# Kernel tuning notes

Hardware: AMD Instinct MI355X
Metric: run time of the kernel (lower is better)

The kernel has to match this reference:

```python
import jax, jax.numpy as jnp
import numpy as np

N = 100000   # nodes
E = 1600000  # edges
EPS = 1e-5   # BatchNorm eps

def setup_inputs() -> dict:
    key = jax.random.key(0)
    ks = jax.random.split(key, 18)
    x = jax.random.normal(ks[0], (N, 128), jnp.float32)
    edge_index = jax.random.randint(ks[1], (2, E), 0, N, dtype=jnp.int64)
    # GCN layer weights (Glorot-ish scale) and biases
    W1 = jax.random.normal(ks[2], (128, 64), jnp.float32) * 0.1
    b1 = jnp.zeros((64,), jnp.float32)
    W2 = jax.random.normal(ks[3], (64, 64), jnp.float32) * 0.1
    b2 = jnp.zeros((64,), jnp.float32)
    W3 = jax.random.normal(ks[4], (64, 16), jnp.float32) * 0.1
    b3 = jnp.zeros((16,), jnp.float32)
    # BatchNorm (eval mode) affine params + running stats, 2 BN layers of width 64
    g1 = jax.random.uniform(ks[5], (64,), jnp.float32, 0.5, 1.5)
    be1 = jax.random.normal(ks[6], (64,), jnp.float32) * 0.1
    m1 = jax.random.normal(ks[7], (64,), jnp.float32) * 0.1
    v1 = jax.random.uniform(ks[8], (64,), jnp.float32, 0.5, 1.5)
    g2 = jax.random.uniform(ks[9], (64,), jnp.float32, 0.5, 1.5)
    be2 = jax.random.normal(ks[10], (64,), jnp.float32) * 0.1
    m2 = jax.random.normal(ks[11], (64,), jnp.float32) * 0.1
    v2 = jax.random.uniform(ks[12], (64,), jnp.float32, 0.5, 1.5)
    return {"x": x, "edge_index": edge_index,
            "W1": W1, "b1": b1, "W2": W2, "b2": b2, "W3": W3, "b3": b3,
            "g1": g1, "be1": be1, "m1": m1, "v1": v1,
            "g2": g2, "be2": be2, "m2": m2, "v2": v2}

def _gcn_graph(edge_index):
    # add self-loops, compute symmetric normalization deg^-1/2 * deg^-1/2
    loop = jnp.arange(N, dtype=edge_index.dtype)
    src = jnp.concatenate([edge_index[0], loop])
    dst = jnp.concatenate([edge_index[1], loop])
    deg = jax.ops.segment_sum(jnp.ones_like(dst, dtype=jnp.float32), dst, num_segments=N)
    dinv = jnp.where(deg > 0, jax.lax.rsqrt(jnp.maximum(deg, 1.0)), 0.0)
    norm = dinv[src] * dinv[dst]  # [E+N]
    return src, dst, norm

def reference(x, edge_index, W1, b1, W2, b2, W3, b3,
              g1, be1, m1, v1, g2, be2, m2, v2):
    src, dst, norm = _gcn_graph(edge_index)

    def conv(h, W, b):
        h = h @ W                              # [N, d_out]
        msg = h[src] * norm[:, None]           # gather + scale, [E+N, d_out]
        return jax.ops.segment_sum(msg, dst, num_segments=N) + b

    def bn(h, g, be, m, v):
        return g * (h - m) * jax.lax.rsqrt(v + EPS) + be

    h = jax.nn.relu(bn(conv(x, W1, b1), g1, be1, m1, v1))
    h = jax.nn.relu(bn(conv(h, W2, b2), g2, be2, m2, v2))
    return jax.nn.sigmoid(conv(h, W3, b3))
```

## Files before the change

kernel.cpp:

```cpp
#include <hip/hip_runtime.h>
#include <math.h>

#define NN 100000
#define NE 1600000
#define EPSBN 1e-5f
#define NBUCK 391

static __device__ __forceinline__ unsigned short f2bf(float f) {
    unsigned int u = __float_as_uint(f);
    u += 0x7fffu + ((u >> 16) & 1u);
    return (unsigned short)(u >> 16);
}
static __device__ __forceinline__ float bf2f(unsigned short s) {
    return __uint_as_float(((unsigned int)s) << 16);
}
static __device__ __forceinline__ float4 bf4_to_f4(ushort4 u) {
    float4 c; c.x = bf2f(u.x); c.y = bf2f(u.y); c.z = bf2f(u.z); c.w = bf2f(u.w);
    return c;
}
static __device__ __forceinline__ void add4(float4& a, float4 c) {
    a.x += c.x; a.y += c.y; a.z += c.z; a.w += c.w;
}
static __device__ __forceinline__ void fma4(float4& a, float s, const float4& w) {
    a.x = fmaf(s, w.x, a.x); a.y = fmaf(s, w.y, a.y);
    a.z = fmaf(s, w.z, a.z); a.w = fmaf(s, w.w, a.w);
}
static __device__ __forceinline__ void fma2(float2& a, float s, const float2& w) {
    a.x = fmaf(s, w.x, a.x); a.y = fmaf(s, w.y, a.y);
}

__global__ __launch_bounds__(512) void init_small(int* __restrict__ bkcnt,
                                                  int* __restrict__ bcur) {
    int t = threadIdx.x;
    bkcnt[t] = 0;
    bcur[t] = 0;
}

__global__ __launch_bounds__(256) void bucket_count(const int* __restrict__ dst,
                                                    int* __restrict__ bkcnt) {
    __shared__ int lh[NBUCK];
    int t = threadIdx.x;
    for (int b = t; b < NBUCK; b += 256) lh[b] = 0;
    __syncthreads();
    int e0 = blockIdx.x * 4096;
#pragma unroll
    for (int i = 0; i < 16; ++i) {
        int e = e0 + i * 256 + t;
        if (e < NE) atomicAdd(&lh[dst[e] >> 8], 1);
    }
    __syncthreads();
    for (int b = t; b < NBUCK; b += 256)
        if (lh[b]) atomicAdd(&bkcnt[b], lh[b]);
}

__global__ __launch_bounds__(512) void scan2(const int* __restrict__ bkcnt,
                                             int* __restrict__ bb0) {
    __shared__ int sh[512];
    int t = threadIdx.x;
    int val = (t < NBUCK) ? bkcnt[t] : 0;
    sh[t] = val;
    __syncthreads();
    for (int off = 1; off < 512; off <<= 1) {
        int x = (t >= off) ? sh[t - off] : 0;
        __syncthreads();
        sh[t] += x;
        __syncthreads();
    }
    bb0[t] = sh[t] - val;
}

__global__ __launch_bounds__(256) void bin_kernel(const int* __restrict__ src,
                                                  const int* __restrict__ dst,
                                                  const int* __restrict__ bb0,
                                                  int* __restrict__ bcur,
                                                  unsigned int* __restrict__ bucketed) {
    __shared__ int lh[NBUCK];
    __shared__ int lbase[NBUCK];
    __shared__ int lcur[NBUCK];
    int t = threadIdx.x;
    for (int b = t; b < NBUCK; b += 256) lh[b] = 0;
    __syncthreads();
    int e0 = blockIdx.x * 4096;
#pragma unroll
    for (int i = 0; i < 16; ++i) {
        int e = e0 + i * 256 + t;
        if (e < NE) atomicAdd(&lh[dst[e] >> 8], 1);
    }
    __syncthreads();
    for (int b = t; b < NBUCK; b += 256) {
        lbase[b] = bb0[b] + atomicAdd(&bcur[b], lh[b]);
        lcur[b] = 0;
    }
    __syncthreads();
#pragma unroll
    for (int i = 0; i < 16; ++i) {
        int e = e0 + i * 256 + t;
        if (e < NE) {
            int d = dst[e], s = src[e];
            int b = d >> 8;
            int pos = lbase[b] + atomicAdd(&lcur[b], 1);
            bucketed[pos] = (unsigned int)s | ((unsigned int)(d & 255) << 24);
        }
    }
}

__global__ __launch_bounds__(256) void fine_scatter_fused(const unsigned int* __restrict__ bucketed,
                                                          const int* __restrict__ bb0,
                                                          int* __restrict__ row_start,
                                                          float* __restrict__ dinv,
                                                          int* __restrict__ sorted_src) {
    __shared__ int hist[256];
    __shared__ int sc[256];
    __shared__ int rsl[256];
    __shared__ int lcur[256];
    int b = blockIdx.x, t = threadIdx.x;
    hist[t] = 0; lcur[t] = 0;
    __syncthreads();
    int e0 = bb0[b], e1 = bb0[b + 1];
    for (int e = e0 + t; e < e1; e += 256)
        atomicAdd(&hist[bucketed[e] >> 24], 1);
    __syncthreads();
    int val = hist[t];
    sc[t] = val;
    __syncthreads();
    for (int off = 1; off < 256; off <<= 1) {
        int x = (t >= off) ? sc[t - off] : 0;
        __syncthreads();
        sc[t] += x;
        __syncthreads();
    }
    int ex = sc[t] - val;
    int node = b * 256 + t;
    if (node < NN) {
        row_start[node] = e0 + ex;
        dinv[node] = rsqrtf(1.0f + (float)val);
    }
    if (node == NN) row_start[NN] = NE;
    rsl[t] = e0 + ex;
    __syncthreads();
    for (int e = e0 + t; e < e1; e += 256) {
        unsigned int p = bucketed[e];
        int dl = (int)(p >> 24);
        int pos = rsl[dl] + atomicAdd(&lcur[dl], 1);
        sorted_src[pos] = (int)(p & 0xFFFFFFu);
    }
}

__global__ __launch_bounds__(256) void gemm_128_64_v3(const float* __restrict__ x,
                                                      const float* __restrict__ W,
                                                      const float* __restrict__ dinv,
                                                      unsigned short* __restrict__ hs) {
    __shared__ float xs[64][132];
    __shared__ float ws[128][64];
    int tid = threadIdx.x;
    int bn = blockIdx.x * 64;
    for (int id = tid; id < 2048; id += 256) {
        int r = id >> 4, c4 = id & 15;
        *(float4*)&ws[r][c4 * 4] = *(const float4*)(W + r * 64 + c4 * 4);
    }
    for (int id = tid; id < 64 * 33; id += 256) {
        int r = id / 33, c4 = id - r * 33;
        int n = bn + r; if (n >= NN) n = NN - 1;
        float4 v = make_float4(0.f, 0.f, 0.f, 0.f);
        if (c4 < 32) v = *(const float4*)(x + (size_t)n * 128 + c4 * 4);
        *(float4*)&xs[r][c4 * 4] = v;
    }
    __syncthreads();
    int tn = tid >> 4, tf = tid & 15;
    int f0 = tf * 4;
    float4 acc[4] = {{0,0,0,0},{0,0,0,0},{0,0,0,0},{0,0,0,0}};
#pragma unroll 2
    for (int k = 0; k < 128; k += 4) {
        float4 w0 = *(const float4*)&ws[k + 0][f0];
        float4 w1 = *(const float4*)&ws[k + 1][f0];
        float4 w2 = *(const float4*)&ws[k + 2][f0];
        float4 w3 = *(const float4*)&ws[k + 3][f0];
#pragma unroll
        for (int i = 0; i < 4; ++i) {
            float4 xa = *(const float4*)&xs[tn * 4 + i][k];
            fma4(acc[i], xa.x, w0); fma4(acc[i], xa.y, w1);
            fma4(acc[i], xa.z, w2); fma4(acc[i], xa.w, w3);
        }
    }
#pragma unroll
    for (int i = 0; i < 4; ++i) {
        int n = bn + tn * 4 + i;
        if (n < NN) {
            float di = dinv[n];
            ushort4 u;
            u.x = f2bf(acc[i].x * di); u.y = f2bf(acc[i].y * di);
            u.z = f2bf(acc[i].z * di); u.w = f2bf(acc[i].w * di);
            *(ushort4*)(hs + (size_t)n * 64 + f0) = u;
        }
    }
}

__global__ __launch_bounds__(256) void gemm_64_64_v3(const float* __restrict__ x,
                                                     const float* __restrict__ W,
                                                     const float* __restrict__ dinv,
                                                     unsigned short* __restrict__ hs) {
    __shared__ float xs[64][68];
    __shared__ float ws[64][64];
    int tid = threadIdx.x;
    int bn = blockIdx.x * 64;
    for (int id = tid; id < 1024; id += 256) {
        int r = id >> 4, c4 = id & 15;
        *(float4*)&ws[r][c4 * 4] = *(const float4*)(W + r * 64 + c4 * 4);
    }
    for (int id = tid; id < 64 * 17; id += 256) {
        int r = id / 17, c4 = id - r * 17;
        int n = bn + r; if (n >= NN) n = NN - 1;
        float4 v = make_float4(0.f, 0.f, 0.f, 0.f);
        if (c4 < 16) v = *(const float4*)(x + (size_t)n * 64 + c4 * 4);
        *(float4*)&xs[r][c4 * 4] = v;
    }
    __syncthreads();
    int tn = tid >> 4, tf = tid & 15;
    int f0 = tf * 4;
    float4 acc[4] = {{0,0,0,0},{0,0,0,0},{0,0,0,0},{0,0,0,0}};
#pragma unroll 2
    for (int k = 0; k < 64; k += 4) {
        float4 w0 = *(const float4*)&ws[k + 0][f0];
        float4 w1 = *(const float4*)&ws[k + 1][f0];
        float4 w2 = *(const float4*)&ws[k + 2][f0];
        float4 w3 = *(const float4*)&ws[k + 3][f0];
#pragma unroll
        for (int i = 0; i < 4; ++i) {
            float4 xa = *(const float4*)&xs[tn * 4 + i][k];
            fma4(acc[i], xa.x, w0); fma4(acc[i], xa.y, w1);
            fma4(acc[i], xa.z, w2); fma4(acc[i], xa.w, w3);
        }
    }
#pragma unroll
    for (int i = 0; i < 4; ++i) {
        int n = bn + tn * 4 + i;
        if (n < NN) {
            float di = dinv[n];
            ushort4 u;
            u.x = f2bf(acc[i].x * di); u.y = f2bf(acc[i].y * di);
            u.z = f2bf(acc[i].z * di); u.w = f2bf(acc[i].w * di);
            *(ushort4*)(hs + (size_t)n * 64 + f0) = u;
        }
    }
}

__global__ __launch_bounds__(256) void gemm_64_16_v3(const float* __restrict__ x,
                                                     const float* __restrict__ W,
                                                     const float* __restrict__ dinv,
                                                     unsigned short* __restrict__ hs) {
    __shared__ float xs[128][68];
    __shared__ float ws[64][16];
    int tid = threadIdx.x;
    int bn = blockIdx.x * 128;
    for (int id = tid; id < 256; id += 256) {
        int r = id >> 2, c4 = id & 3;
        *(float4*)&ws[r][c4 * 4] = *(const float4*)(W + r * 16 + c4 * 4);
    }
    for (int id = tid; id < 128 * 17; id += 256) {
        int r = id / 17, c4 = id - r * 17;
        int n = bn + r; if (n >= NN) n = NN - 1;
        float4 v = make_float4(0.f, 0.f, 0.f, 0.f);
        if (c4 < 16) v = *(const float4*)(x + (size_t)n * 64 + c4 * 4);
        *(float4*)&xs[r][c4 * 4] = v;
    }
    __syncthreads();
    int tn = tid >> 3, tf = tid & 7;
    int f0 = tf * 2;
    float2 acc[4] = {{0,0},{0,0},{0,0},{0,0}};
#pragma unroll 2
    for (int k = 0; k < 64; k += 4) {
        float2 w0 = *(const float2*)&ws[k + 0][f0];
        float2 w1 = *(const float2*)&ws[k + 1][f0];
        float2 w2 = *(const float2*)&ws[k + 2][f0];
        float2 w3 = *(const float2*)&ws[k + 3][f0];
#pragma unroll
        for (int i = 0; i < 4; ++i) {
            float4 xa = *(const float4*)&xs[tn * 4 + i][k];
            fma2(acc[i], xa.x, w0); fma2(acc[i], xa.y, w1);
            fma2(acc[i], xa.z, w2); fma2(acc[i], xa.w, w3);
        }
    }
#pragma unroll
    for (int i = 0; i < 4; ++i) {
        int n = bn + tn * 4 + i;
        if (n < NN) {
            float di = dinv[n];
            ushort2 u;
            u.x = f2bf(acc[i].x * di); u.y = f2bf(acc[i].y * di);
            *(ushort2*)(hs + (size_t)n * 16 + f0) = u;
        }
    }
}

__global__ __launch_bounds__(256) void csr_agg64_v2(const int* __restrict__ rs,
                                                    const int* __restrict__ ss,
                                                    const unsigned short* __restrict__ hs,
                                                    const float* __restrict__ dinv,
                                                    const float* __restrict__ b,
                                                    const float* __restrict__ g,
                                                    const float* __restrict__ be,
                                                    const float* __restrict__ m,
                                                    const float* __restrict__ v,
                                                    float* __restrict__ out) {
    int lane = threadIdx.x & 63;
    int r = blockIdx.x * 4 + (threadIdx.x >> 6);
    int grp = lane >> 4, fl = lane & 15;
    int e0 = rs[r], e1 = rs[r + 1];
    float4 a0 = {0,0,0,0}, a1 = {0,0,0,0}, a2 = {0,0,0,0}, a3 = {0,0,0,0};
    if (grp == 0)
        a0 = bf4_to_f4(*(const ushort4*)(hs + (size_t)r * 64 + fl * 4));
    int jj = e0;
    for (; jj + 16 <= e1; jj += 16) {
        int s0 = ss[jj + grp];
        int s1 = ss[jj + 4 + grp];
        int s2 = ss[jj + 8 + grp];
        int s3 = ss[jj + 12 + grp];
        ushort4 u0 = *(const ushort4*)(hs + (size_t)s0 * 64 + fl * 4);
        ushort4 u1 = *(const ushort4*)(hs + (size_t)s1 * 64 + fl * 4);
        ushort4 u2 = *(const ushort4*)(hs + (size_t)s2 * 64 + fl * 4);
        ushort4 u3 = *(const ushort4*)(hs + (size_t)s3 * 64 + fl * 4);
        add4(a0, bf4_to_f4(u0)); add4(a1, bf4_to_f4(u1));
        add4(a2, bf4_to_f4(u2)); add4(a3, bf4_to_f4(u3));
    }
    for (; jj < e1; jj += 4) {
        int idx = jj + grp;
        if (idx < e1) {
            int s = ss[idx];
            add4(a1, bf4_to_f4(*(const ushort4*)(hs + (size_t)s * 64 + fl * 4)));
        }
    }
    add4(a0, a1); add4(a2, a3); add4(a0, a2);
    a0.x += __shfl_xor(a0.x, 16); a0.y += __shfl_xor(a0.y, 16);
    a0.z += __shfl_xor(a0.z, 16); a0.w += __shfl_xor(a0.w, 16);
    a0.x += __shfl_xor(a0.x, 32); a0.y += __shfl_xor(a0.y, 32);
    a0.z += __shfl_xor(a0.z, 32); a0.w += __shfl_xor(a0.w, 32);
    if (grp == 0) {
        float di = dinv[r];
        float4 bb = *(const float4*)(b + fl * 4);
        float4 gg = *(const float4*)(g + fl * 4);
        float4 bz = *(const float4*)(be + fl * 4);
        float4 mm = *(const float4*)(m + fl * 4);
        float4 vv = *(const float4*)(v + fl * 4);
        float4 h;
        h.x = fmaxf(gg.x * (di * a0.x + bb.x - mm.x) * rsqrtf(vv.x + EPSBN) + bz.x, 0.f);
        h.y = fmaxf(gg.y * (di * a0.y + bb.y - mm.y) * rsqrtf(vv.y + EPSBN) + bz.y, 0.f);
        h.z = fmaxf(gg.z * (di * a0.z + bb.z - mm.z) * rsqrtf(vv.z + EPSBN) + bz.z, 0.f);
        h.w = fmaxf(gg.w * (di * a0.w + bb.w - mm.w) * rsqrtf(vv.w + EPSBN) + bz.w, 0.f);
        *(float4*)(out + (size_t)r * 64 + fl * 4) = h;
    }
}

__global__ __launch_bounds__(256) void csr_agg16_v2(const int* __restrict__ rs,
                                                    const int* __restrict__ ss,
                                                    const unsigned short* __restrict__ hs,
                                                    const float* __restrict__ dinv,
                                                    const float* __restrict__ b,
                                                    float* __restrict__ out) {
    int lane = threadIdx.x & 63;
    int r = blockIdx.x * 4 + (threadIdx.x >> 6);
    int grp = lane >> 3, fl = lane & 7;
    int e0 = rs[r], e1 = rs[r + 1];
    float2 a0 = {0,0}, a1 = {0,0};
    if (grp == 0) {
        ushort2 u = *(const ushort2*)(hs + (size_t)r * 16 + fl * 2);
        a0.x = bf2f(u.x); a0.y = bf2f(u.y);
    }
    int jj = e0;
    for (; jj + 16 <= e1; jj += 16) {
        int s0 = ss[jj + grp];
        int s1 = ss[jj + 8 + grp];
        ushort2 u0 = *(const ushort2*)(hs + (size_t)s0 * 16 + fl * 2);
        ushort2 u1 = *(const ushort2*)(hs + (size_t)s1 * 16 + fl * 2);
        a0.x += bf2f(u0.x); a0.y += bf2f(u0.y);
        a1.x += bf2f(u1.x); a1.y += bf2f(u1.y);
    }
    for (; jj < e1; jj += 8) {
        int idx = jj + grp;
        if (idx < e1) {
            int s = ss[idx];
            ushort2 u = *(const ushort2*)(hs + (size_t)s * 16 + fl * 2);
            a1.x += bf2f(u.x); a1.y += bf2f(u.y);
        }
    }
    a0.x += a1.x; a0.y += a1.y;
    a0.x += __shfl_xor(a0.x, 8);  a0.y += __shfl_xor(a0.y, 8);
    a0.x += __shfl_xor(a0.x, 16); a0.y += __shfl_xor(a0.y, 16);
    a0.x += __shfl_xor(a0.x, 32); a0.y += __shfl_xor(a0.y, 32);
    if (grp == 0) {
        float di = dinv[r];
        float hx = di * a0.x + b[fl * 2];
        float hy = di * a0.y + b[fl * 2 + 1];
        float2 o;
        o.x = 1.0f / (1.0f + expf(-hx));
        o.y = 1.0f / (1.0f + expf(-hy));
        *(float2*)(out + (size_t)r * 16 + fl * 2) = o;
    }
}

extern "C" void kernel_launch(void* const* d_in, const int* in_sizes, int n_in,
                              void* d_out, int out_size, void* d_ws, size_t ws_size,
                              hipStream_t stream) {
    const float* x   = (const float*)d_in[0];
    const int*   ei  = (const int*)d_in[1];
    const float* W1  = (const float*)d_in[2];
    const float* b1  = (const float*)d_in[3];
    const float* W2  = (const float*)d_in[4];
    const float* b2  = (const float*)d_in[5];
    const float* W3  = (const float*)d_in[6];
    const float* b3  = (const float*)d_in[7];
    const float* g1  = (const float*)d_in[8];
    const float* be1 = (const float*)d_in[9];
    const float* m1  = (const float*)d_in[10];
    const float* v1  = (const float*)d_in[11];
    const float* g2  = (const float*)d_in[12];
    const float* be2 = (const float*)d_in[13];
    const float* m2  = (const float*)d_in[14];
    const float* v2  = (const float*)d_in[15];
    float* out = (float*)d_out;

    const int* srcp = ei;
    const int* dstp = ei + NE;

    float* dinv = (float*)d_ws;
    float* A    = dinv + NN;
    unsigned short* Bh = (unsigned short*)(A + (size_t)NN * 64);
    int* row_start  = (int*)(Bh + (size_t)NN * 64);
    int* bkcnt      = row_start + NN + 2;
    int* bb0        = bkcnt + 512;
    int* bcur       = bb0 + 512;
    int* sorted_src = bcur + 512;
    unsigned int* bucketed = (unsigned int*)(sorted_src + NE);

    dim3 blk(256);
    int gBIN  = (NE + 4095) / 4096;
    int gG1   = (NN + 63) / 64;
    int gG3   = (NN + 127) / 128;
    int gA    = NN / 4;

    init_small<<<1, 512, 0, stream>>>(bkcnt, bcur);
    bucket_count<<<gBIN, blk, 0, stream>>>(dstp, bkcnt);
    scan2<<<1, 512, 0, stream>>>(bkcnt, bb0);
    bin_kernel<<<gBIN, blk, 0, stream>>>(srcp, dstp, bb0, bcur, bucketed);
    fine_scatter_fused<<<NBUCK, blk, 0, stream>>>(bucketed, bb0, row_start, dinv, sorted_src);

    gemm_128_64_v3<<<gG1, blk, 0, stream>>>(x, W1, dinv, Bh);
    csr_agg64_v2<<<gA, blk, 0, stream>>>(row_start, sorted_src, Bh, dinv,
                                         b1, g1, be1, m1, v1, A);
    gemm_64_64_v3<<<gG1, blk, 0, stream>>>(A, W2, dinv, Bh);
    csr_agg64_v2<<<gA, blk, 0, stream>>>(row_start, sorted_src, Bh, dinv,
                                         b2, g2, be2, m2, v2, A);
    gemm_64_16_v3<<<gG3, blk, 0, stream>>>(A, W3, dinv, Bh);
    csr_agg16_v2<<<gA, blk, 0, stream>>>(row_start, sorted_src, Bh, dinv, b3, out);
}
```

Before: 379.3 us.

## Store hidden activations in bf16, rework 64-wide aggregation gather, enlarge bin blocks

Intermediate activations between layers are now written and read as bf16 rather than fp32, which halves the traffic for the 64-wide hidden buffers; the follow-on GEMMs convert them back to fp32 when loading into shared memory. The 64-feature CSR aggregation now gives one feature per lane. Each 64-edge chunk of neighbor indices is loaded once and broadcast with shuffles, and 16 independent accumulators keep many gathers in flight. The binning kernel now processes 16K edges per block instead of 4K. The risks are extra rounding error from bf16 activations, 2-byte per-lane gathers that may coalesce less well than the old 8-byte ones, and fewer bin blocks.

Measured after the change: 474.9 us. +25.2%, slower.

```diff
diff --git a/kernel.cpp b/kernel.cpp
--- a/kernel.cpp
+++ b/kernel.cpp
@@ -13,13 +13,6 @@
 }
 static __device__ __forceinline__ float bf2f(unsigned short s) {
     return __uint_as_float(((unsigned int)s) << 16);
-}
-static __device__ __forceinline__ float4 bf4_to_f4(ushort4 u) {
-    float4 c; c.x = bf2f(u.x); c.y = bf2f(u.y); c.z = bf2f(u.z); c.w = bf2f(u.w);
-    return c;
-}
-static __device__ __forceinline__ void add4(float4& a, float4 c) {
-    a.x += c.x; a.y += c.y; a.z += c.z; a.w += c.w;
 }
 static __device__ __forceinline__ void fma4(float4& a, float s, const float4& w) {
     a.x = fmaf(s, w.x, a.x); a.y = fmaf(s, w.y, a.y);
@@ -80,9 +73,9 @@
     int t = threadIdx.x;
     for (int b = t; b < NBUCK; b += 256) lh[b] = 0;
     __syncthreads();
-    int e0 = blockIdx.x * 4096;
-#pragma unroll
-    for (int i = 0; i < 16; ++i) {
+    int e0 = blockIdx.x * 16384;
+#pragma unroll
+    for (int i = 0; i < 64; ++i) {
         int e = e0 + i * 256 + t;
         if (e < NE) atomicAdd(&lh[dst[e] >> 8], 1);
     }
@@ -93,7 +86,7 @@
     }
     __syncthreads();
 #pragma unroll
-    for (int i = 0; i < 16; ++i) {
+    for (int i = 0; i < 64; ++i) {
         int e = e0 + i * 256 + t;
         if (e < NE) {
             int d = dst[e], s = src[e];
@@ -195,7 +188,7 @@
     }
 }
 
-__global__ __launch_bounds__(256) void gemm_64_64_v3(const float* __restrict__ x,
+__global__ __launch_bounds__(256) void gemm_64_64_bf(const unsigned short* __restrict__ xbf,
                                                      const float* __restrict__ W,
                                                      const float* __restrict__ dinv,
                                                      unsigned short* __restrict__ hs) {
@@ -207,11 +200,11 @@
         int r = id >> 4, c4 = id & 15;
         *(float4*)&ws[r][c4 * 4] = *(const float4*)(W + r * 64 + c4 * 4);
     }
-    for (int id = tid; id < 64 * 17; id += 256) {
-        int r = id / 17, c4 = id - r * 17;
+    for (int id = tid; id < 64 * 16; id += 256) {
+        int r = id >> 4, c4 = id & 15;
         int n = bn + r; if (n >= NN) n = NN - 1;
-        float4 v = make_float4(0.f, 0.f, 0.f, 0.f);
-        if (c4 < 16) v = *(const float4*)(x + (size_t)n * 64 + c4 * 4);
+        ushort4 u = *(const ushort4*)(xbf + (size_t)n * 64 + c4 * 4);
+        float4 v; v.x = bf2f(u.x); v.y = bf2f(u.y); v.z = bf2f(u.z); v.w = bf2f(u.w);
         *(float4*)&xs[r][c4 * 4] = v;
     }
     __syncthreads();
@@ -244,7 +237,7 @@
     }
 }
 
-__global__ __launch_bounds__(256) void gemm_64_16_v3(const float* __restrict__ x,
+__global__ __launch_bounds__(256) void gemm_64_16_bf(const unsigned short* __restrict__ xbf,
                                                      const float* __restrict__ W,
                                                      const float* __restrict__ dinv,
                                                      unsigned short* __restrict__ hs) {
@@ -256,11 +249,11 @@
         int r = id >> 2, c4 = id & 3;
         *(float4*)&ws[r][c4 * 4] = *(const float4*)(W + r * 16 + c4 * 4);
     }
-    for (int id = tid; id < 128 * 17; id += 256) {
-        int r = id / 17, c4 = id - r * 17;
+    for (int id = tid; id < 128 * 16; id += 256) {
+        int r = id >> 4, c4 = id & 15;
         int n = bn + r; if (n >= NN) n = NN - 1;
-        float4 v = make_float4(0.f, 0.f, 0.f, 0.f);
-        if (c4 < 16) v = *(const float4*)(x + (size_t)n * 64 + c4 * 4);
+        ushort4 u = *(const ushort4*)(xbf + (size_t)n * 64 + c4 * 4);
+        float4 v; v.x = bf2f(u.x); v.y = bf2f(u.y); v.z = bf2f(u.z); v.w = bf2f(u.w);
         *(float4*)&xs[r][c4 * 4] = v;
     }
     __syncthreads();
@@ -292,7 +285,7 @@
     }
 }
 
-__global__ __launch_bounds__(256) void csr_agg64_v2(const int* __restrict__ rs,
+__global__ __launch_bounds__(256) void csr_agg64_v3(const int* __restrict__ rs,
                                                     const int* __restrict__ ss,
                                                     const unsigned short* __restrict__ hs,
                                                     const float* __restrict__ dinv,
@@ -301,53 +294,32 @@
                                                     const float* __restrict__ be,
                                                     const float* __restrict__ m,
                                                     const float* __restrict__ v,
-                                                    float* __restrict__ out) {
+                                                    unsigned short* __restrict__ outbf) {
     int lane = threadIdx.x & 63;
     int r = blockIdx.x * 4 + (threadIdx.x >> 6);
-    int grp = lane >> 4, fl = lane & 15;
     int e0 = rs[r], e1 = rs[r + 1];
-    float4 a0 = {0,0,0,0}, a1 = {0,0,0,0}, a2 = {0,0,0,0}, a3 = {0,0,0,0};
-    if (grp == 0)
-        a0 = bf4_to_f4(*(const ushort4*)(hs + (size_t)r * 64 + fl * 4));
-    int jj = e0;
-    for (; jj + 16 <= e1; jj += 16) {
-        int s0 = ss[jj + grp];
-        int s1 = ss[jj + 4 + grp];
-        int s2 = ss[jj + 8 + grp];
-        int s3 = ss[jj + 12 + grp];
-        ushort4 u0 = *(const ushort4*)(hs + (size_t)s0 * 64 + fl * 4);
-        ushort4 u1 = *(const ushort4*)(hs + (size_t)s1 * 64 + fl * 4);
-        ushort4 u2 = *(const ushort4*)(hs + (size_t)s2 * 64 + fl * 4);
-        ushort4 u3 = *(const ushort4*)(hs + (size_t)s3 * 64 + fl * 4);
-        add4(a0, bf4_to_f4(u0)); add4(a1, bf4_to_f4(u1));
-        add4(a2, bf4_to_f4(u2)); add4(a3, bf4_to_f4(u3));
-    }
-    for (; jj < e1; jj += 4) {
-        int idx = jj + grp;
-        if (idx < e1) {
-            int s = ss[idx];
-            add4(a1, bf4_to_f4(*(const ushort4*)(hs + (size_t)s * 64 + fl * 4)));
-        }
-    }
-    add4(a0, a1); add4(a2, a3); add4(a0, a2);
-    a0.x += __shfl_xor(a0.x, 16); a0.y += __shfl_xor(a0.y, 16);
-    a0.z += __shfl_xor(a0.z, 16); a0.w += __shfl_xor(a0.w, 16);
-    a0.x += __shfl_xor(a0.x, 32); a0.y += __shfl_xor(a0.y, 32);
-    a0.z += __shfl_xor(a0.z, 32); a0.w += __shfl_xor(a0.w, 32);
-    if (grp == 0) {
-        float di = dinv[r];
-        float4 bb = *(const float4*)(b + fl * 4);
-        float4 gg = *(const float4*)(g + fl * 4);
-        float4 bz = *(const float4*)(be + fl * 4);
-        float4 mm = *(const float4*)(m + fl * 4);
-        float4 vv = *(const float4*)(v + fl * 4);
-        float4 h;
-        h.x = fmaxf(gg.x * (di * a0.x + bb.x - mm.x) * rsqrtf(vv.x + EPSBN) + bz.x, 0.f);
-        h.y = fmaxf(gg.y * (di * a0.y + bb.y - mm.y) * rsqrtf(vv.y + EPSBN) + bz.y, 0.f);
-        h.z = fmaxf(gg.z * (di * a0.z + bb.z - mm.z) * rsqrtf(vv.z + EPSBN) + bz.z, 0.f);
-        h.w = fmaxf(gg.w * (di * a0.w + bb.w - mm.w) * rsqrtf(vv.w + EPSBN) + bz.w, 0.f);
-        *(float4*)(out + (size_t)r * 64 + fl * 4) = h;
-    }
+    float a0 = bf2f(hs[(size_t)r * 64 + lane]);
+    float a1 = 0.f, a2 = 0.f, a3 = 0.f, a4 = 0.f, a5 = 0.f, a6 = 0.f, a7 = 0.f;
+    float a8 = 0.f, a9 = 0.f, a10 = 0.f, a11 = 0.f, a12 = 0.f, a13 = 0.f, a14 = 0.f, a15 = 0.f;
+    for (int base = e0; base < e1; base += 64) {
+        int nbb = e1 - base; if (nbb > 64) nbb = 64;
+        int sidx = (lane < nbb) ? ss[base + lane] : 0;
+        for (int j = 0; j < nbb; j += 16) {
+#define GATH(K, ACC) if (j + K < nbb) { \
+    int s_ = __shfl(sidx, j + K); \
+    ACC += bf2f(hs[(size_t)s_ * 64 + lane]); }
+            GATH(0, a0)  GATH(1, a1)  GATH(2, a2)  GATH(3, a3)
+            GATH(4, a4)  GATH(5, a5)  GATH(6, a6)  GATH(7, a7)
+            GATH(8, a8)  GATH(9, a9)  GATH(10, a10) GATH(11, a11)
+            GATH(12, a12) GATH(13, a13) GATH(14, a14) GATH(15, a15)
+#undef GATH
+        }
+    }
+    float acc = ((a0 + a1) + (a2 + a3)) + ((a4 + a5) + (a6 + a7))
+              + ((a8 + a9) + (a10 + a11)) + ((a12 + a13) + (a14 + a15));
+    float h = dinv[r] * acc + b[lane];
+    h = g[lane] * (h - m[lane]) * rsqrtf(v[lane] + EPSBN) + be[lane];
+    outbf[(size_t)r * 64 + lane] = f2bf(fmaxf(h, 0.f));
 }
 
 __global__ __launch_bounds__(256) void csr_agg16_v2(const int* __restrict__ rs,
@@ -422,8 +394,8 @@
     const int* dstp = ei + NE;
 
     float* dinv = (float*)d_ws;
-    float* A    = dinv + NN;
-    unsigned short* Bh = (unsigned short*)(A + (size_t)NN * 64);
+    unsigned short* Abf = (unsigned short*)(dinv + NN);
+    unsigned short* Bh  = Abf + (size_t)NN * 64;
     int* row_start  = (int*)(Bh + (size_t)NN * 64);
     int* bkcnt      = row_start + NN + 2;
     int* bb0        = bkcnt + 512;
@@ -432,23 +404,24 @@
     unsigned int* bucketed = (unsigned int*)(sorted_src + NE);
 
     dim3 blk(256);
-    int gBIN  = (NE + 4095) / 4096;
+    int gCNT  = (NE + 4095) / 4096;
+    int gBIN  = (NE + 16383) / 16384;
     int gG1   = (NN + 63) / 64;
     int gG3   = (NN + 127) / 128;
     int gA    = NN / 4;
 
     init_small<<<1, 512, 0, stream>>>(bkcnt, bcur);
-    bucket_count<<<gBIN, blk, 0, stream>>>(dstp, bkcnt);
+    bucket_count<<<gCNT, blk, 0, stream>>>(dstp, bkcnt);
     scan2<<<1, 512, 0, stream>>>(bkcnt, bb0);
     bin_kernel<<<gBIN, blk, 0, stream>>>(srcp, dstp, bb0, bcur, bucketed);
     fine_scatter_fused<<<NBUCK, blk, 0, stream>>>(bucketed, bb0, row_start, dinv, sorted_src);
 
     gemm_128_64_v3<<<gG1, blk, 0, stream>>>(x, W1, dinv, Bh);
-    csr_agg64_v2<<<gA, blk, 0, stream>>>(row_start, sorted_src, Bh, dinv,
-                                         b1, g1, be1, m1, v1, A);
-    gemm_64_64_v3<<<gG1, blk, 0, stream>>>(A, W2, dinv, Bh);
-    csr_agg64_v2<<<gA, blk, 0, stream>>>(row_start, sorted_src, Bh, dinv,
-                                         b2, g2, be2, m2, v2, A);
-    gemm_64_16_v3<<<gG3, blk, 0, stream>>>(A, W3, dinv, Bh);
+    csr_agg64_v3<<<gA, blk, 0, stream>>>(row_start, sorted_src, Bh, dinv,
+                                         b1, g1, be1, m1, v1, Abf);
+    gemm_64_64_bf<<<gG1, blk, 0, stream>>>(Abf, W2, dinv, Bh);
+    csr_agg64_v3<<<gA, blk, 0, stream>>>(row_start, sorted_src, Bh, dinv,
+                                         b2, g2, be2, m2, v2, Abf);
+    gemm_64_16_bf<<<gG3, blk, 0, stream>>>(Abf, W3, dinv, Bh);
     csr_agg16_v2<<<gA, blk, 0, stream>>>(row_start, sorted_src, Bh, dinv, b3, out);
 }
```
